# Kernel tuning notes

Measured on AMD Instinct MI355X. Metric: run time of the kernel, lower is better.

Reference implementation:

```python
import jax, jax.numpy as jnp
import numpy as np

T, B, I, H = 512, 64, 1024, 1024


def _lstm_scan(x, h0, c0, w_ih, w_hh, b, reverse):
    # x: [T,B,I]; standard LSTM gate order (i,f,g,o)
    def step(carry, xt):
        h, c = carry
        gates = xt @ w_ih.T + h @ w_hh.T + b  # [B,4H]
        i_g, f_g, g_g, o_g = jnp.split(gates, 4, axis=-1)
        c = jax.nn.sigmoid(f_g) * c + jax.nn.sigmoid(i_g) * jnp.tanh(g_g)
        h = jax.nn.sigmoid(o_g) * jnp.tanh(c)
        return (h, c), h
    (h, c), ys = jax.lax.scan(step, (h0, c0), x, reverse=reverse)
    return ys, h, c


def setup_inputs() -> dict:
    key = jax.random.key(0)
    ks = jax.random.split(key, 13)
    s = 1.0 / np.sqrt(H)
    return {
        "x": jax.random.normal(ks[0], (T, B, I), jnp.float32),
        "h0_f": jax.random.normal(ks[1], (B, H), jnp.float32),
        "c0_f": jax.random.normal(ks[2], (B, H), jnp.float32),
        "h0_b": jax.random.normal(ks[3], (B, H), jnp.float32),
        "c0_b": jax.random.normal(ks[4], (B, H), jnp.float32),
        "w_ih_f": jax.random.normal(ks[5], (4 * H, I), jnp.float32) * s,
        "w_hh_f": jax.random.normal(ks[6], (4 * H, H), jnp.float32) * s,
        "b_ih_f": jax.random.normal(ks[7], (4 * H,), jnp.float32) * s,
        "b_hh_f": jax.random.normal(ks[8], (4 * H,), jnp.float32) * s,
        "w_ih_b": jax.random.normal(ks[9], (4 * H, I), jnp.float32) * s,
        "w_hh_b": jax.random.normal(ks[10], (4 * H, H), jnp.float32) * s,
        "b_ih_b": jax.random.normal(ks[11], (4 * H,), jnp.float32) * s,
        "b_hh_b": jax.random.normal(ks[12], (4 * H,), jnp.float32) * s,
    }


def reference(x, h0_f, c0_f, h0_b, c0_b,
              w_ih_f, w_hh_f, b_ih_f, b_hh_f,
              w_ih_b, w_hh_b, b_ih_b, b_hh_b):
    # forward direction
    ys_f, hT_f, cT_f = _lstm_scan(x, h0_f, c0_f, w_ih_f, w_hh_f,
                                  b_ih_f + b_hh_f, reverse=False)
    # reverse direction (process time reversed, outputs re-reversed by scan)
    ys_b, hT_b, cT_b = _lstm_scan(x, h0_b, c0_b, w_ih_b, w_hh_b,
                                  b_ih_b + b_hh_b, reverse=True)
    out = jnp.concatenate([ys_f, ys_b], axis=-1)  # [T,B,2H]
    return (out, hT_f, cT_f, hT_b, cT_b)
```

## Files before the change

kernel.cpp:

```cpp
#include <hip/hip_runtime.h>
#include <math.h>

#define T_DIM 512
#define B_DIM 64
#define I_DIM 1024
#define H_DIM 1024

#define OUT_HTF (T_DIM * B_DIM * 2 * H_DIM)
#define OUT_CTF (OUT_HTF + B_DIM * H_DIM)
#define OUT_HTB (OUT_CTF + B_DIM * H_DIM)
#define OUT_CTB (OUT_HTB + B_DIM * H_DIM)

__device__ __forceinline__ float sigmoidf_(float v) {
    return 1.0f / (1.0f + expf(-v));
}

__global__ __launch_bounds__(256) void lstm_step(
    const float* __restrict__ x,
    const float* __restrict__ h0f, const float* __restrict__ c0f,
    const float* __restrict__ h0b, const float* __restrict__ c0b,
    const float* __restrict__ wihf, const float* __restrict__ whhf,
    const float* __restrict__ bihf, const float* __restrict__ bhhf,
    const float* __restrict__ wihb, const float* __restrict__ whhb,
    const float* __restrict__ bihb, const float* __restrict__ bhhb,
    float* __restrict__ out, int step)
{
    __shared__ float smem[2 * 64 * 128];

    const int tid = threadIdx.x;
    const int bid = blockIdx.x;
    const int dir = bid >> 7;
    const int u0  = (bid & 127) * 8;
    const int t   = dir ? (T_DIM - 1 - step) : step;

    const float* w_ih = dir ? wihb : wihf;
    const float* w_hh = dir ? whhb : whhf;
    const float* xt   = x + (size_t)t * B_DIM * I_DIM;

    const float* hprev;
    int hst;
    if (step == 0) {
        hprev = dir ? h0b : h0f;
        hst = H_DIM;
    } else {
        const int tprev = dir ? (t + 1) : (t - 1);
        hprev = out + (size_t)tprev * B_DIM * 2 * H_DIM + dir * H_DIM;
        hst = 2 * H_DIM;
    }

    const int jp = tid >> 4;
    const int mg = tid & 15;
    const int c0 = jp * 2;
    const int j0 = (c0 >> 3) * H_DIM + u0 + (c0 & 7);

    float acc[4][2];
#pragma unroll
    for (int i = 0; i < 4; ++i) { acc[i][0] = 0.f; acc[i][1] = 0.f; }

    float4 ld[8];

    auto issue_loads = [&](int kc) {
        const bool isX = (kc < 8);
        const float* src = isX ? xt : hprev;
        const int stride = isX ? I_DIM : hst;
        const int kb = (isX ? kc : (kc - 8)) * 128;
#pragma unroll
        for (int p = 0; p < 8; ++p) {
            const int e = p * 256 + tid;
            const int m = e >> 5;
            const int q = e & 31;
            ld[p] = *reinterpret_cast<const float4*>(
                src + (size_t)m * stride + kb + q * 4);
        }
    };

    auto write_smem = [&](int buf) {
        float* dst = smem + buf * 8192;
#pragma unroll
        for (int p = 0; p < 8; ++p) {
            const int e = p * 256 + tid;
            const int m = e >> 5;
            const int q = e & 31;
            const int qs = q ^ ((m >> 2) & 7);
            *reinterpret_cast<float4*>(&dst[m * 128 + qs * 4]) = ld[p];
        }
    };

    auto compute = [&](int kc, int buf) {
        const bool isX = (kc < 8);
        const int kb = (isX ? kc : (kc - 8)) * 128;
        const float* wp0 = (isX ? w_ih : w_hh) + (size_t)j0 * 1024 + kb;
        const float* wp1 = wp0 + 1024;
        const float* sb = smem + buf * 8192 + (mg * 4) * 128;
#pragma unroll 4
        for (int q = 0; q < 32; ++q) {
            const float4 w0 = *reinterpret_cast<const float4*>(wp0 + q * 4);
            const float4 w1 = *reinterpret_cast<const float4*>(wp1 + q * 4);
            const int qs = (q ^ (mg & 7)) * 4;
#pragma unroll
            for (int i = 0; i < 4; ++i) {
                const float4 a =
                    *reinterpret_cast<const float4*>(&sb[i * 128 + qs]);
                acc[i][0] = fmaf(a.x, w0.x, fmaf(a.y, w0.y,
                            fmaf(a.z, w0.z, fmaf(a.w, w0.w, acc[i][0]))));
                acc[i][1] = fmaf(a.x, w1.x, fmaf(a.y, w1.y,
                            fmaf(a.z, w1.z, fmaf(a.w, w1.w, acc[i][1]))));
            }
        }
    };

    issue_loads(0);
    write_smem(0);
    __syncthreads();
    for (int kc = 0; kc < 16; ++kc) {
        if (kc < 15) issue_loads(kc + 1);
        compute(kc, kc & 1);
        __syncthreads();
        if (kc < 15) {
            write_smem((kc + 1) & 1);
            __syncthreads();
        }
    }

    const float* bih = dir ? bihb : bihf;
    const float* bhh = dir ? bhhb : bhhf;
    const float bb0 = bih[j0] + bhh[j0];
    const float bb1 = bih[j0 + 1] + bhh[j0 + 1];

#pragma unroll
    for (int i = 0; i < 4; ++i) {
        const int m = mg * 4 + i;
        smem[c0 * 65 + m]       = acc[i][0] + bb0;
        smem[(c0 + 1) * 65 + m] = acc[i][1] + bb1;
    }
    __syncthreads();

    float* cslot = out + (dir ? OUT_CTB : OUT_CTF);
    float* hslot = out + (dir ? OUT_HTB : OUT_HTF);
    const float* cinit = dir ? c0b : c0f;
#pragma unroll
    for (int s2 = 0; s2 < 2; ++s2) {
        const int cell = s2 * 256 + tid;
        const int du = cell >> 6;
        const int m = cell & 63;
        const int u = u0 + du;
        const float ig = smem[(0 * 8 + du) * 65 + m];
        const float fg = smem[(1 * 8 + du) * 65 + m];
        const float gg = smem[(2 * 8 + du) * 65 + m];
        const float og = smem[(3 * 8 + du) * 65 + m];
        const float cp = (step == 0) ? cinit[m * H_DIM + u]
                                     : cslot[m * H_DIM + u];
        const float cn = sigmoidf_(fg) * cp + sigmoidf_(ig) * tanhf(gg);
        const float h  = sigmoidf_(og) * tanhf(cn);
        cslot[m * H_DIM + u] = cn;
        out[(size_t)t * B_DIM * 2 * H_DIM + m * 2 * H_DIM + dir * H_DIM + u] = h;
        if (step == T_DIM - 1) hslot[m * H_DIM + u] = h;
    }
}

extern "C" void kernel_launch(void* const* d_in, const int* in_sizes, int n_in,
                              void* d_out, int out_size, void* d_ws, size_t ws_size,
                              hipStream_t stream)
{
    const float* x    = (const float*)d_in[0];
    const float* h0f  = (const float*)d_in[1];
    const float* c0f  = (const float*)d_in[2];
    const float* h0b  = (const float*)d_in[3];
    const float* c0b  = (const float*)d_in[4];
    const float* wihf = (const float*)d_in[5];
    const float* whhf = (const float*)d_in[6];
    const float* bihf = (const float*)d_in[7];
    const float* bhhf = (const float*)d_in[8];
    const float* wihb = (const float*)d_in[9];
    const float* whhb = (const float*)d_in[10];
    const float* bihb = (const float*)d_in[11];
    const float* bhhb = (const float*)d_in[12];
    float* out = (float*)d_out;

    for (int s = 0; s < T_DIM; ++s) {
        lstm_step<<<dim3(256), dim3(256), 0, stream>>>(
            x, h0f, c0f, h0b, c0b,
            wihf, whhf, bihf, bhhf,
            wihb, whhb, bihb, bhhb,
            out, s);
    }
}
```

Baseline: 50.08 ms.

## Hoist input projection into one batched GEMM before the recurrent step loop

Precomputes x@W_ih^T plus biases for all timesteps and both directions in a single large GEMM written to workspace. The per-step kernel then only does the h@W_hh^T product, split across twice as many blocks by halving the batch per block. This takes the input-projection work off the serial critical path. It needs 1 GiB of fp32 workspace, falls back to bf16 storage (which loses precision) when only half that is available, and keeps the old monolithic kernel when workspace is smaller still.

```diff
diff --git a/kernel.cpp b/kernel.cpp
--- a/kernel.cpp
+++ b/kernel.cpp
@@ -1,4 +1,5 @@
 #include <hip/hip_runtime.h>
+#include <hip/hip_bf16.h>
 #include <math.h>
 
 #define T_DIM 512
@@ -15,7 +16,259 @@
     return 1.0f / (1.0f + expf(-v));
 }
 
-__global__ __launch_bounds__(256) void lstm_step(
+template <typename GT>
+__device__ __forceinline__ float4 load4g(const GT* p) {
+    if constexpr (sizeof(GT) == 4) {
+        return *reinterpret_cast<const float4*>(p);
+    } else {
+        const __hip_bfloat16* b = reinterpret_cast<const __hip_bfloat16*>(p);
+        __hip_bfloat16 tmp[4];
+        *reinterpret_cast<uint2*>(tmp) = *reinterpret_cast<const uint2*>(b);
+        return make_float4(__bfloat162float(tmp[0]), __bfloat162float(tmp[1]),
+                           __bfloat162float(tmp[2]), __bfloat162float(tmp[3]));
+    }
+}
+
+template <typename GT>
+__device__ __forceinline__ void store8g(GT* p, const float* v) {
+    if constexpr (sizeof(GT) == 4) {
+        *reinterpret_cast<float4*>(p)     = make_float4(v[0], v[1], v[2], v[3]);
+        *reinterpret_cast<float4*>(p + 4) = make_float4(v[4], v[5], v[6], v[7]);
+    } else {
+        __hip_bfloat16 tmp[8];
+#pragma unroll
+        for (int i = 0; i < 8; ++i) tmp[i] = __float2bfloat16(v[i]);
+        *reinterpret_cast<float4*>(p) = *reinterpret_cast<float4*>(tmp);
+    }
+}
+
+template <typename GT>
+__global__ __launch_bounds__(256) void xproj_gemm(
+    const float* __restrict__ x,
+    const float* __restrict__ wihf, const float* __restrict__ bihf,
+    const float* __restrict__ bhhf,
+    const float* __restrict__ wihb, const float* __restrict__ bihb,
+    const float* __restrict__ bhhb,
+    GT* __restrict__ gx)
+{
+    __shared__ float smem[2 * 64 * 128];
+
+    const int tid = threadIdx.x;
+    const int nb  = blockIdx.x;
+    const int dir = nb >> 5;
+    const int n0  = (nb & 31) * 128;
+    const int m0  = blockIdx.y * 64;
+
+    const float* w  = dir ? wihb : wihf;
+    const float* bi = dir ? bihb : bihf;
+    const float* bh = dir ? bhhb : bhhf;
+    const float* A  = x + (size_t)m0 * I_DIM;
+
+    const int jp = tid >> 4;
+    const int mg = tid & 15;
+    const int j0 = n0 + jp * 8;
+
+    float acc[4][8] = {};
+    float4 ld[8];
+
+    auto issue_loads = [&](int kc) {
+        const int kb = kc * 128;
+#pragma unroll
+        for (int p = 0; p < 8; ++p) {
+            const int e = p * 256 + tid;
+            const int m = e >> 5;
+            const int q = e & 31;
+            ld[p] = *reinterpret_cast<const float4*>(A + (size_t)m * I_DIM + kb + q * 4);
+        }
+    };
+    auto write_smem = [&](int buf) {
+        float* dst = smem + buf * 8192;
+#pragma unroll
+        for (int p = 0; p < 8; ++p) {
+            const int e = p * 256 + tid;
+            const int m = e >> 5;
+            const int q = e & 31;
+            const int qs = q ^ ((m >> 2) & 7);
+            *reinterpret_cast<float4*>(&dst[m * 128 + qs * 4]) = ld[p];
+        }
+    };
+    auto compute = [&](int kc, int buf) {
+        const int kb = kc * 128;
+        const float* wp = w + (size_t)j0 * 1024 + kb;
+        const float* sb = smem + buf * 8192 + (mg * 4) * 128;
+#pragma unroll 2
+        for (int q = 0; q < 32; ++q) {
+            const int qs = (q ^ (mg & 7)) * 4;
+            float4 a[4];
+#pragma unroll
+            for (int i = 0; i < 4; ++i)
+                a[i] = *reinterpret_cast<const float4*>(&sb[i * 128 + qs]);
+#pragma unroll
+            for (int cj = 0; cj < 8; ++cj) {
+                const float4 wv =
+                    *reinterpret_cast<const float4*>(wp + (size_t)cj * 1024 + q * 4);
+#pragma unroll
+                for (int i = 0; i < 4; ++i) {
+                    acc[i][cj] = fmaf(a[i].x, wv.x, fmaf(a[i].y, wv.y,
+                                 fmaf(a[i].z, wv.z, fmaf(a[i].w, wv.w, acc[i][cj]))));
+                }
+            }
+        }
+    };
+
+    issue_loads(0);
+    write_smem(0);
+    __syncthreads();
+    for (int kc = 0; kc < 8; ++kc) {
+        if (kc < 7) issue_loads(kc + 1);
+        compute(kc, kc & 1);
+        __syncthreads();
+        if (kc < 7) {
+            write_smem((kc + 1) & 1);
+            __syncthreads();
+        }
+    }
+
+    float bias[8];
+#pragma unroll
+    for (int cj = 0; cj < 8; ++cj) bias[cj] = bi[j0 + cj] + bh[j0 + cj];
+
+    GT* gbase = gx + (size_t)dir * (32768ull * 4096ull);
+#pragma unroll
+    for (int i = 0; i < 4; ++i) {
+        const int row = m0 + mg * 4 + i;
+        float v[8];
+#pragma unroll
+        for (int cj = 0; cj < 8; ++cj) v[cj] = acc[i][cj] + bias[cj];
+        store8g(gbase + (size_t)row * 4096 + j0, v);
+    }
+}
+
+template <typename GT>
+__global__ __launch_bounds__(256) void lstm_step_h(
+    const float* __restrict__ h0f, const float* __restrict__ c0f,
+    const float* __restrict__ h0b, const float* __restrict__ c0b,
+    const float* __restrict__ whhf, const float* __restrict__ whhb,
+    const GT* __restrict__ gx,
+    float* __restrict__ out, int step)
+{
+    __shared__ float smem[2 * 32 * 128];
+
+    const int tid = threadIdx.x;
+    const int bid = blockIdx.x;
+    const int dir = bid >> 8;
+    const int mh  = (bid >> 7) & 1;
+    const int u0  = (bid & 127) * 8;
+    const int t   = dir ? (T_DIM - 1 - step) : step;
+    const int m0  = mh * 32;
+
+    const float* whh = dir ? whhb : whhf;
+
+    const float* hprev;
+    int hst;
+    if (step == 0) {
+        hprev = dir ? h0b : h0f;
+        hst = H_DIM;
+    } else {
+        const int tprev = dir ? (t + 1) : (t - 1);
+        hprev = out + (size_t)tprev * B_DIM * 2 * H_DIM + dir * H_DIM;
+        hst = 2 * H_DIM;
+    }
+
+    const int jp = tid >> 5;
+    const int mg = tid & 31;
+    const int j_base = (jp >> 1) * H_DIM + u0 + (jp & 1) * 4;
+
+    float acc[4] = {0.f, 0.f, 0.f, 0.f};
+    float4 ld[4];
+
+    auto issue_loads = [&](int kc) {
+        const int kb = kc * 128;
+#pragma unroll
+        for (int p = 0; p < 4; ++p) {
+            const int e = p * 256 + tid;
+            const int m = e >> 5;
+            const int q = e & 31;
+            ld[p] = *reinterpret_cast<const float4*>(
+                hprev + (size_t)(m0 + m) * hst + kb + q * 4);
+        }
+    };
+    auto write_smem = [&](int buf) {
+        float* dst = smem + buf * 4096;
+#pragma unroll
+        for (int p = 0; p < 4; ++p) {
+            const int e = p * 256 + tid;
+            const int m = e >> 5;
+            const int q = e & 31;
+            const int qs = q ^ ((m >> 2) & 7);
+            *reinterpret_cast<float4*>(&dst[m * 128 + qs * 4]) = ld[p];
+        }
+    };
+    auto compute = [&](int kc, int buf) {
+        const int kb = kc * 128;
+        const float* wp = whh + (size_t)j_base * 1024 + kb;
+        const float* sb = smem + buf * 4096 + mg * 128;
+#pragma unroll 4
+        for (int q = 0; q < 32; ++q) {
+            const int qs = (q ^ ((mg >> 2) & 7)) * 4;
+            const float4 a = *reinterpret_cast<const float4*>(&sb[qs]);
+#pragma unroll
+            for (int ci = 0; ci < 4; ++ci) {
+                const float4 wv =
+                    *reinterpret_cast<const float4*>(wp + (size_t)ci * 1024 + q * 4);
+                acc[ci] = fmaf(a.x, wv.x, fmaf(a.y, wv.y,
+                          fmaf(a.z, wv.z, fmaf(a.w, wv.w, acc[ci]))));
+            }
+        }
+    };
+
+    issue_loads(0);
+    write_smem(0);
+    __syncthreads();
+    for (int kc = 0; kc < 8; ++kc) {
+        if (kc < 7) issue_loads(kc + 1);
+        compute(kc, kc & 1);
+        __syncthreads();
+        if (kc < 7) {
+            write_smem((kc + 1) & 1);
+            __syncthreads();
+        }
+    }
+
+    const GT* gsl = gx + (size_t)dir * (32768ull * 4096ull)
+                    + (size_t)(t * 64 + m0 + mg) * 4096 + j_base;
+    const float4 gxv = load4g(gsl);
+
+    const int c0 = jp * 4;
+    smem[(c0 + 0) * 33 + mg] = acc[0] + gxv.x;
+    smem[(c0 + 1) * 33 + mg] = acc[1] + gxv.y;
+    smem[(c0 + 2) * 33 + mg] = acc[2] + gxv.z;
+    smem[(c0 + 3) * 33 + mg] = acc[3] + gxv.w;
+    __syncthreads();
+
+    const int du = tid >> 5;
+    const int m  = tid & 31;
+    const int b  = m0 + m;
+    const int u  = u0 + du;
+
+    const float ig = smem[(0 * 8 + du) * 33 + m];
+    const float fg = smem[(1 * 8 + du) * 33 + m];
+    const float gg = smem[(2 * 8 + du) * 33 + m];
+    const float og = smem[(3 * 8 + du) * 33 + m];
+
+    float* cslot = out + (dir ? OUT_CTB : OUT_CTF);
+    float* hslot = out + (dir ? OUT_HTB : OUT_HTF);
+    const float* cinit = dir ? c0b : c0f;
+
+    const float cp = (step == 0) ? cinit[b * H_DIM + u] : cslot[b * H_DIM + u];
+    const float cn = sigmoidf_(fg) * cp + sigmoidf_(ig) * tanhf(gg);
+    const float h  = sigmoidf_(og) * tanhf(cn);
+    cslot[b * H_DIM + u] = cn;
+    out[(size_t)t * B_DIM * 2 * H_DIM + b * 2 * H_DIM + dir * H_DIM + u] = h;
+    if (step == T_DIM - 1) hslot[b * H_DIM + u] = h;
+}
+
+__global__ __launch_bounds__(256) void lstm_step_mono(
     const float* __restrict__ x,
     const float* __restrict__ h0f, const float* __restrict__ c0f,
     const float* __restrict__ h0b, const float* __restrict__ c0b,
@@ -73,7 +326,6 @@
                 src + (size_t)m * stride + kb + q * 4);
         }
     };
-
     auto write_smem = [&](int buf) {
         float* dst = smem + buf * 8192;
 #pragma unroll
@@ -85,7 +337,6 @@
             *reinterpret_cast<float4*>(&dst[m * 128 + qs * 4]) = ld[p];
         }
     };
-
     auto compute = [&](int kc, int buf) {
         const bool isX = (kc < 8);
         const int kb = (isX ? kc : (kc - 8)) * 128;
@@ -177,11 +428,33 @@
     const float* bhhb = (const float*)d_in[12];
     float* out = (float*)d_out;
 
-    for (int s = 0; s < T_DIM; ++s) {
-        lstm_step<<<dim3(256), dim3(256), 0, stream>>>(
-            x, h0f, c0f, h0b, c0b,
-            wihf, whhf, bihf, bhhf,
-            wihb, whhb, bihb, bhhb,
-            out, s);
-    }
-}
+    const size_t GX_ELEMS = 2ull * 32768ull * 4096ull;
+    const size_t NEED_F32 = GX_ELEMS * 4ull;
+    const size_t NEED_B16 = GX_ELEMS * 2ull;
+
+    if (ws_size >= NEED_F32) {
+        float* gx = (float*)d_ws;
+        xproj_gemm<float><<<dim3(64, 512), 256, 0, stream>>>(
+            x, wihf, bihf, bhhf, wihb, bihb, bhhb, gx);
+        for (int s = 0; s < T_DIM; ++s) {
+            lstm_step_h<float><<<dim3(512), 256, 0, stream>>>(
+                h0f, c0f, h0b, c0b, whhf, whhb, gx, out, s);
+        }
+    } else if (ws_size >= NEED_B16) {
+        __hip_bfloat16* gx = (__hip_bfloat16*)d_ws;
+        xproj_gemm<__hip_bfloat16><<<dim3(64, 512), 256, 0, stream>>>(
+            x, wihf, bihf, bhhf, wihb, bihb, bhhb, gx);
+        for (int s = 0; s < T_DIM; ++s) {
+            lstm_step_h<__hip_bfloat16><<<dim3(512), 256, 0, stream>>>(
+                h0f, c0f, h0b, c0b, whhf, whhb, gx, out, s);
+        }
+    } else {
+        for (int s = 0; s < T_DIM; ++s) {
+            lstm_step_mono<<<dim3(256), dim3(256), 0, stream>>>(
+                x, h0f, c0f, h0b, c0b,
+                wihf, whhf, bihf, bhhf,
+                wihb, whhb, bihb, bhhb,
+                out, s);
+        }
+    }
+}
```

Measured after the change: 54.81 ms. 1.09x slower.

## Remap LSTM step threads so each wave shares weight rows across batch lanes

Applied to the files above, without the earlier changes.

Changes the thread-to-output mapping so that each wave owns one gate and eight hidden units, and each lane owns one batch row. All lanes in a wave now read the same weight addresses, which can become broadcast or even scalar loads, while each lane reads only its own activation row from shared memory with an XOR swizzle. The bias is folded into the accumulator initialisation and the epilogue shared-memory layout is rearranged to match. The trade-off is eight weight vector loads per shared-memory load instead of the previous balance, and a strided epilogue read that may cause bank conflicts.

```diff
diff --git a/kernel.cpp b/kernel.cpp
--- a/kernel.cpp
+++ b/kernel.cpp
@@ -15,7 +15,7 @@
     return 1.0f / (1.0f + expf(-v));
 }
 
-__global__ __launch_bounds__(256) void lstm_step(
+__global__ __launch_bounds__(256, 1) void lstm_step_fused(
     const float* __restrict__ x,
     const float* __restrict__ h0f, const float* __restrict__ c0f,
     const float* __restrict__ h0b, const float* __restrict__ c0b,
@@ -27,14 +27,18 @@
 {
     __shared__ float smem[2 * 64 * 128];
 
-    const int tid = threadIdx.x;
-    const int bid = blockIdx.x;
-    const int dir = bid >> 7;
-    const int u0  = (bid & 127) * 8;
-    const int t   = dir ? (T_DIM - 1 - step) : step;
+    const int tid  = threadIdx.x;
+    const int bid  = blockIdx.x;
+    const int dir  = bid >> 7;
+    const int u0   = (bid & 127) * 8;
+    const int t    = dir ? (T_DIM - 1 - step) : step;
+    const int lane = tid & 63;
+    const int g    = tid >> 6;
 
     const float* w_ih = dir ? wihb : wihf;
     const float* w_hh = dir ? whhb : whhf;
+    const float* bih  = dir ? bihb : bihf;
+    const float* bhh  = dir ? bhhb : bhhf;
     const float* xt   = x + (size_t)t * B_DIM * I_DIM;
 
     const float* hprev;
@@ -48,14 +52,11 @@
         hst = 2 * H_DIM;
     }
 
-    const int jp = tid >> 4;
-    const int mg = tid & 15;
-    const int c0 = jp * 2;
-    const int j0 = (c0 >> 3) * H_DIM + u0 + (c0 & 7);
+    const int row0 = g * H_DIM + u0;
 
-    float acc[4][2];
+    float acc[8];
 #pragma unroll
-    for (int i = 0; i < 4; ++i) { acc[i][0] = 0.f; acc[i][1] = 0.f; }
+    for (int ci = 0; ci < 8; ++ci) acc[ci] = bih[row0 + ci] + bhh[row0 + ci];
 
     float4 ld[8];
 
@@ -63,7 +64,7 @@
         const bool isX = (kc < 8);
         const float* src = isX ? xt : hprev;
         const int stride = isX ? I_DIM : hst;
-        const int kb = (isX ? kc : (kc - 8)) * 128;
+        const int kb = (kc & 7) * 128;
 #pragma unroll
         for (int p = 0; p < 8; ++p) {
             const int e = p * 256 + tid;
@@ -81,30 +82,26 @@
             const int e = p * 256 + tid;
             const int m = e >> 5;
             const int q = e & 31;
-            const int qs = q ^ ((m >> 2) & 7);
+            const int qs = q ^ (m & 31);
             *reinterpret_cast<float4*>(&dst[m * 128 + qs * 4]) = ld[p];
         }
     };
 
     auto compute = [&](int kc, int buf) {
         const bool isX = (kc < 8);
-        const int kb = (isX ? kc : (kc - 8)) * 128;
-        const float* wp0 = (isX ? w_ih : w_hh) + (size_t)j0 * 1024 + kb;
-        const float* wp1 = wp0 + 1024;
-        const float* sb = smem + buf * 8192 + (mg * 4) * 128;
+        const int kb = (kc & 7) * 128;
+        const float* wb = (isX ? w_ih : w_hh) + (size_t)row0 * 1024 + kb;
+        const float* sb = smem + buf * 8192 + lane * 128;
+        const int msw = lane & 31;
 #pragma unroll 4
         for (int q = 0; q < 32; ++q) {
-            const float4 w0 = *reinterpret_cast<const float4*>(wp0 + q * 4);
-            const float4 w1 = *reinterpret_cast<const float4*>(wp1 + q * 4);
-            const int qs = (q ^ (mg & 7)) * 4;
+            const float4 a = *reinterpret_cast<const float4*>(&sb[(q ^ msw) * 4]);
 #pragma unroll
-            for (int i = 0; i < 4; ++i) {
-                const float4 a =
-                    *reinterpret_cast<const float4*>(&sb[i * 128 + qs]);
-                acc[i][0] = fmaf(a.x, w0.x, fmaf(a.y, w0.y,
-                            fmaf(a.z, w0.z, fmaf(a.w, w0.w, acc[i][0]))));
-                acc[i][1] = fmaf(a.x, w1.x, fmaf(a.y, w1.y,
-                            fmaf(a.z, w1.z, fmaf(a.w, w1.w, acc[i][1]))));
+            for (int ci = 0; ci < 8; ++ci) {
+                const float4 wv =
+                    *reinterpret_cast<const float4*>(wb + (size_t)ci * 1024 + q * 4);
+                acc[ci] = fmaf(a.x, wv.x, fmaf(a.y, wv.y,
+                          fmaf(a.z, wv.z, fmaf(a.w, wv.w, acc[ci]))));
             }
         }
     };
@@ -122,17 +119,9 @@
         }
     }
 
-    const float* bih = dir ? bihb : bihf;
-    const float* bhh = dir ? bhhb : bhhf;
-    const float bb0 = bih[j0] + bhh[j0];
-    const float bb1 = bih[j0 + 1] + bhh[j0 + 1];
-
 #pragma unroll
-    for (int i = 0; i < 4; ++i) {
-        const int m = mg * 4 + i;
-        smem[c0 * 65 + m]       = acc[i][0] + bb0;
-        smem[(c0 + 1) * 65 + m] = acc[i][1] + bb1;
-    }
+    for (int ci = 0; ci < 8; ++ci)
+        smem[g * 512 + ci * 64 + lane] = acc[ci];
     __syncthreads();
 
     float* cslot = out + (dir ? OUT_CTB : OUT_CTF);
@@ -140,21 +129,23 @@
     const float* cinit = dir ? c0b : c0f;
 #pragma unroll
     for (int s2 = 0; s2 < 2; ++s2) {
-        const int cell = s2 * 256 + tid;
-        const int du = cell >> 6;
-        const int m = cell & 63;
-        const int u = u0 + du;
-        const float ig = smem[(0 * 8 + du) * 65 + m];
-        const float fg = smem[(1 * 8 + du) * 65 + m];
-        const float gg = smem[(2 * 8 + du) * 65 + m];
-        const float og = smem[(3 * 8 + du) * 65 + m];
-        const float cp = (step == 0) ? cinit[m * H_DIM + u]
-                                     : cslot[m * H_DIM + u];
+        const int idx = s2 * 256 + tid;
+        const int u = idx & 7;
+        const int m = idx >> 3;
+        const int uu = u0 + u;
+
+        const float ig = smem[0 * 512 + u * 64 + m];
+        const float fg = smem[1 * 512 + u * 64 + m];
+        const float gg = smem[2 * 512 + u * 64 + m];
+        const float og = smem[3 * 512 + u * 64 + m];
+
+        const float cp = (step == 0) ? cinit[m * H_DIM + uu]
+                                     : cslot[m * H_DIM + uu];
         const float cn = sigmoidf_(fg) * cp + sigmoidf_(ig) * tanhf(gg);
         const float h  = sigmoidf_(og) * tanhf(cn);
-        cslot[m * H_DIM + u] = cn;
-        out[(size_t)t * B_DIM * 2 * H_DIM + m * 2 * H_DIM + dir * H_DIM + u] = h;
-        if (step == T_DIM - 1) hslot[m * H_DIM + u] = h;
+        cslot[m * H_DIM + uu] = cn;
+        out[(size_t)t * B_DIM * 2 * H_DIM + m * 2 * H_DIM + dir * H_DIM + uu] = h;
+        if (step == T_DIM - 1) hslot[m * H_DIM + uu] = h;
     }
 }
 
@@ -178,7 +169,7 @@
     float* out = (float*)d_out;
 
     for (int s = 0; s < T_DIM; ++s) {
-        lstm_step<<<dim3(256), dim3(256), 0, stream>>>(
+        lstm_step_fused<<<dim3(256), dim3(256), 0, stream>>>(
             x, h0f, c0f, h0b, c0b,
             wihf, whhf, bihf, bhhf,
             wihb, whhb, bihb, bhhb,
```

Measured after the change: 97.70 ms. 1.95x slower.
